# Optimization experiments

Measured on AMD Instinct MI355X. Metric: run time of the kernel, lower is better.

## Reference

```python
import jax, jax.numpy as jnp
import numpy as np

B, N_VERT, N_TRI = 64, 50000, 100000

def setup_inputs() -> dict:
    key = jax.random.key(0)
    k1, k2 = jax.random.split(key)
    x = jax.random.normal(k1, (B, N_VERT * 3), dtype=jnp.float32)
    M = jax.random.randint(k2, (N_TRI, 3), 0, N_VERT, dtype=jnp.int64)
    return {"x": x, "M": M}

def reference(x, M):
    temp_shape = x.shape
    xv = x.reshape(x.shape[0], -1, 3)            # [B, N, 3]
    tri = xv[:, M]                               # [B, T, 3, 3] gather triangle vertices
    v0, v1, v2 = tri[:, :, 0], tri[:, :, 1], tri[:, :, 2]
    det = jnp.sum(v0 * jnp.cross(v1, v2), axis=-1)   # [B, T]
    vol = jnp.sum(jnp.abs(det), axis=1) / 6.0        # [B]
    scale = vol ** (1.0 / 3.0)                       # [B]
    out = xv / scale[:, None, None]
    return out.reshape(temp_shape)
```

## Files before the change

kernel.cpp:

```cpp
#include <hip/hip_runtime.h>
#include <hip/hip_fp16.h>

#define NBATCH 64
#define NV 50000
#define NT 100000
#define FPB (NV * 3)

typedef float f32x4 __attribute__((ext_vector_type(4)));
typedef int i32x4 __attribute__((ext_vector_type(4)));


#define GWAVES 4096
#define NGROUP (NT / 8)
#define XH_HALVES ((size_t)FPB * NBATCH)
#define WS_NEED (XH_HALVES * 2 + (size_t)GWAVES * NBATCH * 8 + 256)

__global__ __launch_bounds__(256) void transpose_kernel(
    const float* __restrict__ x, __half* __restrict__ xH) {
  __shared__ float tile[64][65];
  const int tx = threadIdx.x & 63;
  const int ty = threadIdx.x >> 6;
  const int f0 = blockIdx.x * 64;
  const int fl = f0 + tx;
  #pragma unroll
  for (int i = ty; i < 64; i += 4) {
    if (fl < FPB) tile[i][tx] = x[(size_t)i * FPB + fl];
  }
  __syncthreads();
  #pragma unroll
  for (int i = ty; i < 64; i += 4) {
    const int f = f0 + i;
    if (f < FPB) {
      const int v = f / 3, c = f - 3 * v;
      xH[((size_t)c * NV + v) * 64 + tx] = __float2half(tile[tx][i]);
    }
  }
}

__device__ __forceinline__ float hext(const i32x4& v, int j) {
  const int word = v[j >> 1];
  const __half2 h = __builtin_bit_cast(__half2, word);
  return (j & 1) ? __high2float(h) : __low2float(h);
}

__global__ __launch_bounds__(256) void gather_det8_kernel(
    const __half* __restrict__ xH, const int* __restrict__ M,
    double* __restrict__ partials) {
  const int w = blockIdx.x * 4 + (threadIdx.x >> 6);
  const int lane = threadIdx.x & 63;
  const int sub = lane >> 3;
  const int boct = lane & 7;
  const __half* __restrict__ pX = xH;
  const __half* __restrict__ pY = xH + (size_t)NV * 64;
  const __half* __restrict__ pZ = xH + (size_t)2 * NV * 64;
  const size_t o = 8 * boct;

  double acc[8];
  #pragma unroll
  for (int j = 0; j < 8; ++j) acc[j] = 0.0;

  for (int g = w; g < NGROUP; g += GWAVES) {
    const int t = g * 8 + sub;
    const int i0 = M[3 * t + 0];
    const int i1 = M[3 * t + 1];
    const int i2 = M[3 * t + 2];
    const i32x4 A0 = *(const i32x4*)(pX + (size_t)i0 * 64 + o);
    const i32x4 A1 = *(const i32x4*)(pY + (size_t)i0 * 64 + o);
    const i32x4 A2 = *(const i32x4*)(pZ + (size_t)i0 * 64 + o);
    const i32x4 B0 = *(const i32x4*)(pX + (size_t)i1 * 64 + o);
    const i32x4 B1 = *(const i32x4*)(pY + (size_t)i1 * 64 + o);
    const i32x4 B2 = *(const i32x4*)(pZ + (size_t)i1 * 64 + o);
    const i32x4 C0 = *(const i32x4*)(pX + (size_t)i2 * 64 + o);
    const i32x4 C1 = *(const i32x4*)(pY + (size_t)i2 * 64 + o);
    const i32x4 C2 = *(const i32x4*)(pZ + (size_t)i2 * 64 + o);
    #pragma unroll
    for (int j = 0; j < 8; ++j) {
      const float a0 = hext(A0, j), a1 = hext(A1, j), a2 = hext(A2, j);
      const float b0 = hext(B0, j), b1 = hext(B1, j), b2 = hext(B2, j);
      const float c0 = hext(C0, j), c1 = hext(C1, j), c2 = hext(C2, j);
      const float det = a0 * (b1 * c2 - b2 * c1) +
                        a1 * (b2 * c0 - b0 * c2) +
                        a2 * (b0 * c1 - b1 * c0);
      acc[j] += (double)fabsf(det);
    }
  }
  #pragma unroll
  for (int j = 0; j < 8; ++j) {
    acc[j] += __shfl_xor(acc[j], 8, 64);
    acc[j] += __shfl_xor(acc[j], 16, 64);
    acc[j] += __shfl_xor(acc[j], 32, 64);
  }
  if (sub == 0) {
    #pragma unroll
    for (int j = 0; j < 8; ++j)
      partials[(size_t)w * NBATCH + boct * 8 + j] = acc[j];
  }
}

__global__ __launch_bounds__(256) void finalize_t_kernel(
    const double* __restrict__ partials, float* __restrict__ inv_scale) {
  const int b = blockIdx.x;
  double acc = 0.0;
  for (int w = threadIdx.x; w < GWAVES; w += 256)
    acc += partials[(size_t)w * NBATCH + b];
  #pragma unroll
  for (int off = 32; off > 0; off >>= 1) acc += __shfl_down(acc, off, 64);
  __shared__ double lds[4];
  const int lane = threadIdx.x & 63;
  const int wave = threadIdx.x >> 6;
  if (lane == 0) lds[wave] = acc;
  __syncthreads();
  if (threadIdx.x == 0) {
    const double vol = ((lds[0] + lds[1]) + (lds[2] + lds[3])) / 6.0;
    inv_scale[b] = (float)(1.0 / cbrt(vol));
  }
}


#define XCDS 8
#define SLOTS 256
#define GRID_VOL (XCDS * SLOTS)
#define BATCH_PER_XCD (NBATCH / XCDS)

__global__ __launch_bounds__(256) void vol_partial_kernel(
    const float* __restrict__ x, const int* __restrict__ M,
    double* __restrict__ partials) {
  const int L = blockIdx.x;
  const int xcd = L & (XCDS - 1);
  const int slot = L >> 3;
  __shared__ double lds[4];
  const int lane = threadIdx.x & 63;
  const int wave = threadIdx.x >> 6;
  for (int bi = 0; bi < BATCH_PER_XCD; ++bi) {
    const int b = xcd * BATCH_PER_XCD + bi;
    const float* __restrict__ xv = x + (size_t)b * FPB;
    double acc = 0.0;
    for (int t = slot * 256 + threadIdx.x; t < NT; t += SLOTS * 256) {
      const int i0 = M[3 * t + 0], i1 = M[3 * t + 1], i2 = M[3 * t + 2];
      const float a0 = xv[3 * i0], a1 = xv[3 * i0 + 1], a2 = xv[3 * i0 + 2];
      const float b0 = xv[3 * i1], b1 = xv[3 * i1 + 1], b2 = xv[3 * i1 + 2];
      const float c0 = xv[3 * i2], c1 = xv[3 * i2 + 1], c2 = xv[3 * i2 + 2];
      const float det = a0 * (b1 * c2 - b2 * c1) + a1 * (b2 * c0 - b0 * c2) +
                        a2 * (b0 * c1 - b1 * c0);
      acc += (double)fabsf(det);
    }
    #pragma unroll
    for (int off = 32; off > 0; off >>= 1) acc += __shfl_down(acc, off, 64);
    if (lane == 0) lds[wave] = acc;
    __syncthreads();
    if (threadIdx.x == 0)
      partials[(size_t)b * SLOTS + slot] = (lds[0] + lds[1]) + (lds[2] + lds[3]);
    __syncthreads();
  }
}

__global__ __launch_bounds__(256) void finalize_kernel(
    const double* __restrict__ partials, float* __restrict__ inv_scale) {
  const int b = blockIdx.x;
  double v = partials[(size_t)b * SLOTS + threadIdx.x];
  #pragma unroll
  for (int off = 32; off > 0; off >>= 1) v += __shfl_down(v, off, 64);
  __shared__ double lds[4];
  const int lane = threadIdx.x & 63;
  const int wave = threadIdx.x >> 6;
  if (lane == 0) lds[wave] = v;
  __syncthreads();
  if (threadIdx.x == 0) {
    const double vol = ((lds[0] + lds[1]) + (lds[2] + lds[3])) / 6.0;
    inv_scale[b] = (float)(1.0 / cbrt(vol));
  }
}


__global__ __launch_bounds__(256) void normalize_kernel(
    const float* __restrict__ x, const float* __restrict__ inv_scale,
    float* __restrict__ out) {
  const int b = blockIdx.y;
  const float s = inv_scale[b];
  const f32x4* __restrict__ xin =
      reinterpret_cast<const f32x4*>(x + (size_t)b * FPB);
  f32x4* __restrict__ o = reinterpret_cast<f32x4*>(out + (size_t)b * FPB);
  const int n4 = FPB / 4;
  const int stride = blockDim.x * gridDim.x;
  for (int i = blockIdx.x * blockDim.x + threadIdx.x; i < n4; i += stride) {
    f32x4 v = xin[i];
    v *= s;
    __builtin_nontemporal_store(v, &o[i]);
  }
}

extern "C" void kernel_launch(void* const* d_in, const int* in_sizes, int n_in,
                              void* d_out, int out_size, void* d_ws, size_t ws_size,
                              hipStream_t stream) {
  const float* x = (const float*)d_in[0];
  const int* M = (const int*)d_in[1];
  float* out = (float*)d_out;

  float* inv_scale;
  if (ws_size >= WS_NEED) {
    __half* xH = (__half*)d_ws;
    double* partials = (double*)((char*)d_ws + XH_HALVES * 2);
    inv_scale = (float*)(partials + (size_t)GWAVES * NBATCH);

    const int ntiles = (FPB + 63) / 64;
    transpose_kernel<<<ntiles, 256, 0, stream>>>(x, xH);
    gather_det8_kernel<<<GWAVES / 4, 256, 0, stream>>>(xH, M, partials);
    finalize_t_kernel<<<NBATCH, 256, 0, stream>>>(partials, inv_scale);
  } else {
    double* partials = (double*)d_ws;
    inv_scale = (float*)(partials + NBATCH * SLOTS);
    vol_partial_kernel<<<GRID_VOL, 256, 0, stream>>>(x, M, partials);
    finalize_kernel<<<NBATCH, SLOTS, 0, stream>>>(partials, inv_scale);
  }

  dim3 gridC(32, NBATCH);
  normalize_kernel<<<gridC, 256, 0, stream>>>(x, inv_scale, out);
}
```

Measured before the change: 60.07 us.

## Fuse volume finalize into normalize and reduce gather partials per block

The gather kernel now reduces its four waves' partial sums in shared memory and writes one per-block partial per batch in batch-major layout. The grid grows from 1024 to 2048 blocks. The separate finalize kernel is removed: every normalize block re-reduces the 2048 partials for its batch, computes the inverse cube-root scale, and scales its chunk. This drops one kernel launch and the inv_scale round trip, at the cost of redundant per-block reductions (16 blocks per batch each read 16KB of partials).

```diff
diff --git a/kernel.cpp b/kernel.cpp
--- a/kernel.cpp
+++ b/kernel.cpp
@@ -5,15 +5,27 @@
 #define NV 50000
 #define NT 100000
 #define FPB (NV * 3)
+#define N4 (FPB / 4)
+
+#define NTILES ((FPB + 63) / 64)
+#define GBLOCKS 2048
+#define GWAVES (GBLOCKS * 4)
+#define NGROUP (NT / 8)
+#define NCHUNK 16
+#define CHUNK ((N4 + NCHUNK - 1) / NCHUNK)
+
+#define XH_HALVES ((size_t)FPB * NBATCH)
+#define XH_BYTES (XH_HALVES * 2)
+#define WS_NEED (XH_BYTES + (size_t)NBATCH * GBLOCKS * 8 + 256)
 
 typedef float f32x4 __attribute__((ext_vector_type(4)));
 typedef int i32x4 __attribute__((ext_vector_type(4)));
 
-
-#define GWAVES 4096
-#define NGROUP (NT / 8)
-#define XH_HALVES ((size_t)FPB * NBATCH)
-#define WS_NEED (XH_HALVES * 2 + (size_t)GWAVES * NBATCH * 8 + 256)
+__device__ __forceinline__ float hext(const i32x4& v, int j) {
+  const int word = v[j >> 1];
+  const __half2 h = __builtin_bit_cast(__half2, word);
+  return (j & 1) ? __high2float(h) : __low2float(h);
+}
 
 __global__ __launch_bounds__(256) void transpose_kernel(
     const float* __restrict__ x, __half* __restrict__ xH) {
@@ -23,9 +35,8 @@
   const int f0 = blockIdx.x * 64;
   const int fl = f0 + tx;
   #pragma unroll
-  for (int i = ty; i < 64; i += 4) {
+  for (int i = ty; i < 64; i += 4)
     if (fl < FPB) tile[i][tx] = x[(size_t)i * FPB + fl];
-  }
   __syncthreads();
   #pragma unroll
   for (int i = ty; i < 64; i += 4) {
@@ -37,23 +48,19 @@
   }
 }
 
-__device__ __forceinline__ float hext(const i32x4& v, int j) {
-  const int word = v[j >> 1];
-  const __half2 h = __builtin_bit_cast(__half2, word);
-  return (j & 1) ? __high2float(h) : __low2float(h);
-}
-
 __global__ __launch_bounds__(256) void gather_det8_kernel(
     const __half* __restrict__ xH, const int* __restrict__ M,
     double* __restrict__ partials) {
-  const int w = blockIdx.x * 4 + (threadIdx.x >> 6);
-  const int lane = threadIdx.x & 63;
-  const int sub = lane >> 3;
-  const int boct = lane & 7;
+  const int ty = threadIdx.x >> 6;
+  const int tx = threadIdx.x & 63;
+  const int w = blockIdx.x * 4 + ty;
+  const int sub = tx >> 3;
+  const int boct = tx & 7;
   const __half* __restrict__ pX = xH;
   const __half* __restrict__ pY = xH + (size_t)NV * 64;
   const __half* __restrict__ pZ = xH + (size_t)2 * NV * 64;
   const size_t o = 8 * boct;
+  __shared__ double red[4][64];
 
   double acc[8];
   #pragma unroll
@@ -92,34 +99,49 @@
   }
   if (sub == 0) {
     #pragma unroll
-    for (int j = 0; j < 8; ++j)
-      partials[(size_t)w * NBATCH + boct * 8 + j] = acc[j];
-  }
-}
-
-__global__ __launch_bounds__(256) void finalize_t_kernel(
-    const double* __restrict__ partials, float* __restrict__ inv_scale) {
-  const int b = blockIdx.x;
-  double acc = 0.0;
-  for (int w = threadIdx.x; w < GWAVES; w += 256)
-    acc += partials[(size_t)w * NBATCH + b];
-  #pragma unroll
-  for (int off = 32; off > 0; off >>= 1) acc += __shfl_down(acc, off, 64);
-  __shared__ double lds[4];
-  const int lane = threadIdx.x & 63;
-  const int wave = threadIdx.x >> 6;
-  if (lane == 0) lds[wave] = acc;
-  __syncthreads();
-  if (threadIdx.x == 0) {
-    const double vol = ((lds[0] + lds[1]) + (lds[2] + lds[3])) / 6.0;
-    inv_scale[b] = (float)(1.0 / cbrt(vol));
+    for (int j = 0; j < 8; ++j) red[ty][boct * 8 + j] = acc[j];
+  }
+  __syncthreads();
+  if (ty == 0) {
+    const double s = ((red[0][tx] + red[1][tx]) + (red[2][tx] + red[3][tx]));
+    partials[(size_t)tx * GBLOCKS + blockIdx.x] = s;
+  }
+}
+
+__global__ __launch_bounds__(256) void normfin_kernel(
+    const float* __restrict__ x, const double* __restrict__ partials,
+    float* __restrict__ out) {
+  const int batch = blockIdx.x >> 4;
+  const int chunk = blockIdx.x & (NCHUNK - 1);
+  const int tid = threadIdx.x;
+  const int tx = tid & 63;
+  const int ty = tid >> 6;
+  __shared__ double red[4];
+
+  const double* __restrict__ pb = partials + (size_t)batch * GBLOCKS;
+  double local = 0.0;
+  #pragma unroll
+  for (int k = 0; k < GBLOCKS / 256; ++k) local += pb[tid + k * 256];
+  #pragma unroll
+  for (int off = 32; off > 0; off >>= 1) local += __shfl_down(local, off, 64);
+  if (tx == 0) red[ty] = local;
+  __syncthreads();
+  const double vol = ((red[0] + red[1]) + (red[2] + red[3])) / 6.0;
+  const float s = (float)(1.0 / cbrt(vol));
+
+  const f32x4* __restrict__ xb = (const f32x4*)(x + (size_t)batch * FPB);
+  f32x4* __restrict__ ob = (f32x4*)(out + (size_t)batch * FPB);
+  const int i1 = min((chunk + 1) * CHUNK, N4);
+  for (int i = chunk * CHUNK + tid; i < i1; i += 256) {
+    f32x4 v = xb[i];
+    v *= s;
+    __builtin_nontemporal_store(v, &ob[i]);
   }
 }
 
 
 #define XCDS 8
 #define SLOTS 256
-#define GRID_VOL (XCDS * SLOTS)
 #define BATCH_PER_XCD (NBATCH / XCDS)
 
 __global__ __launch_bounds__(256) void vol_partial_kernel(
@@ -171,7 +193,6 @@
   }
 }
 
-
 __global__ __launch_bounds__(256) void normalize_kernel(
     const float* __restrict__ x, const float* __restrict__ inv_scale,
     float* __restrict__ out) {
@@ -180,9 +201,8 @@
   const f32x4* __restrict__ xin =
       reinterpret_cast<const f32x4*>(x + (size_t)b * FPB);
   f32x4* __restrict__ o = reinterpret_cast<f32x4*>(out + (size_t)b * FPB);
-  const int n4 = FPB / 4;
   const int stride = blockDim.x * gridDim.x;
-  for (int i = blockIdx.x * blockDim.x + threadIdx.x; i < n4; i += stride) {
+  for (int i = blockIdx.x * blockDim.x + threadIdx.x; i < N4; i += stride) {
     f32x4 v = xin[i];
     v *= s;
     __builtin_nontemporal_store(v, &o[i]);
@@ -196,23 +216,18 @@
   const int* M = (const int*)d_in[1];
   float* out = (float*)d_out;
 
-  float* inv_scale;
   if (ws_size >= WS_NEED) {
     __half* xH = (__half*)d_ws;
-    double* partials = (double*)((char*)d_ws + XH_HALVES * 2);
-    inv_scale = (float*)(partials + (size_t)GWAVES * NBATCH);
-
-    const int ntiles = (FPB + 63) / 64;
-    transpose_kernel<<<ntiles, 256, 0, stream>>>(x, xH);
-    gather_det8_kernel<<<GWAVES / 4, 256, 0, stream>>>(xH, M, partials);
-    finalize_t_kernel<<<NBATCH, 256, 0, stream>>>(partials, inv_scale);
+    double* partials = (double*)((char*)d_ws + XH_BYTES);
+    transpose_kernel<<<NTILES, 256, 0, stream>>>(x, xH);
+    gather_det8_kernel<<<GBLOCKS, 256, 0, stream>>>(xH, M, partials);
+    normfin_kernel<<<NBATCH * NCHUNK, 256, 0, stream>>>(x, partials, out);
   } else {
     double* partials = (double*)d_ws;
-    inv_scale = (float*)(partials + NBATCH * SLOTS);
-    vol_partial_kernel<<<GRID_VOL, 256, 0, stream>>>(x, M, partials);
+    float* inv_scale = (float*)(partials + NBATCH * SLOTS);
+    vol_partial_kernel<<<XCDS * SLOTS, 256, 0, stream>>>(x, M, partials);
     finalize_kernel<<<NBATCH, SLOTS, 0, stream>>>(partials, inv_scale);
-  }
-
-  dim3 gridC(32, NBATCH);
-  normalize_kernel<<<gridC, 256, 0, stream>>>(x, inv_scale, out);
-}
+    dim3 gridC(32, NBATCH);
+    normalize_kernel<<<gridC, 256, 0, stream>>>(x, inv_scale, out);
+  }
+}
```

Result: faster. 53.80 us (-10.4%).
